# Optimization experiments

Hardware: AMD Instinct MI355X
Metric: run time of the kernel (lower is better)

Reference implementation:

```python
import jax, jax.numpy as jnp
import numpy as np

B, N, CIN, CD, NE = 64, 256, 768, 32, 8192

def setup_inputs() -> dict:
    key = jax.random.key(0)
    ks = jax.random.split(key, 8)
    z = jax.random.normal(ks[0], (B, N, CIN), dtype=jnp.float32)
    # Embedding weight: trunc_normal_(mean=0, std=1, a=-3, b=3)
    emb_weight = jax.random.truncated_normal(ks[1], -3.0, 3.0, (NE, CD)).astype(jnp.float32)
    # Linears stored as [in, out] so y = x @ W + b
    W_compress = jax.random.normal(ks[2], (CIN, CD), dtype=jnp.float32) / np.sqrt(CIN)
    b_compress = jnp.zeros((CD,), dtype=jnp.float32)
    W_ct = jax.random.normal(ks[3], (CD, CD), dtype=jnp.float32) / np.sqrt(CD)
    b_ct = jnp.zeros((CD,), dtype=jnp.float32)
    W_expand = jax.random.normal(ks[4], (CD, CIN), dtype=jnp.float32) / np.sqrt(CD)
    b_expand = jnp.zeros((CIN,), dtype=jnp.float32)
    return {"z": z, "emb_weight": emb_weight, "W_compress": W_compress,
            "b_compress": b_compress, "W_ct": W_ct, "b_ct": b_ct,
            "W_expand": W_expand, "b_expand": b_expand}

def reference(z, emb_weight, W_compress, b_compress, W_ct, b_ct, W_expand, b_expand):
    sg = jax.lax.stop_gradient
    # torch uses embedding.weight.data -> detached codebook input
    implicit_codebook = sg(emb_weight) @ W_ct + b_ct              # [NE, CD]
    zc = z @ W_compress + b_compress                              # [B, N, CD]
    z_flat = zc.reshape(-1, zc.shape[-1])                         # [B*N, CD]
    # squared distance: ||z||^2 + ||c||^2 - 2 z.c
    d = (jnp.sum(z_flat ** 2, axis=1, keepdims=True)
         + jnp.sum(implicit_codebook ** 2, axis=1)
         - 2.0 * jnp.einsum('bd,nd->bn', z_flat, implicit_codebook))  # [B*N, NE]
    indices = jnp.argmin(d, axis=1)                               # [B*N]
    z_q = implicit_codebook[indices]                              # [B*N, CD]
    # training-path losses (codebook + 2.0 * commitment)
    loss = (jnp.mean((sg(z_q) - z_flat) ** 2)
            + 2.0 * jnp.mean((z_q - sg(z_flat)) ** 2))
    # straight-through estimator
    z_st = sg(z_q) + z_flat - sg(z_flat)
    out = z_st.reshape(zc.shape) @ W_expand + b_expand            # [B, N, CIN]
    return out, loss
```

## Files before the change

kernel.cpp:

```cpp
#include <hip/hip_runtime.h>

constexpr int CIN = 768;
constexpr int CD  = 32;
constexpr int NE  = 8192;
constexpr int M   = 16384;
constexpr int SCH = 64;
constexpr int CPC = NE / SCH;
constexpr int PTB = 128;
#define MARGIN 0.05f

typedef short short8 __attribute__((ext_vector_type(8)));
typedef float f32x4  __attribute__((ext_vector_type(4)));

__device__ inline void split_bf16(float x, unsigned short& h, unsigned short& l) {
  unsigned u = __float_as_uint(x);
  unsigned hb = (u + 0x7FFFu + ((u >> 16) & 1u)) >> 16;
  float hf = __uint_as_float(hb << 16);
  float r = x - hf;
  unsigned u2 = __float_as_uint(r);
  unsigned lb = (u2 + 0x7FFFu + ((u2 >> 16) & 1u)) >> 16;
  h = (unsigned short)hb;
  l = (unsigned short)lb;
}

__device__ inline void gload_lds16(const void* g, void* l) {
  __builtin_amdgcn_global_load_lds(
      (const __attribute__((address_space(1))) unsigned int*)g,
      (__attribute__((address_space(3))) unsigned int*)l, 16, 0, 0);
}

__global__ __launch_bounds__(256) void k_split(
    const float* __restrict__ Wc, const float* __restrict__ We,
    unsigned short* __restrict__ WcTh, unsigned short* __restrict__ WcTl,
    unsigned short* __restrict__ WeTh, unsigned short* __restrict__ WeTl) {
  const int t = threadIdx.x;
  if (blockIdx.x < 96) {
    const int idx = blockIdx.x * 256 + t;
    const int k = idx >> 5, n = idx & 31;
    unsigned short h, l;
    split_bf16(Wc[idx], h, l);
    WcTh[n * CIN + k] = h;
    WcTl[n * CIN + k] = l;
  } else {
    const int idx = (blockIdx.x - 96) * 256 + t;
    const int k = idx / CIN, n = idx - k * CIN;
    unsigned short h, l;
    split_bf16(We[idx], h, l);
    WeTh[n * CD + k] = h;
    WeTl[n * CD + k] = l;
  }
}

__global__ __launch_bounds__(256) void k_main(
    const float* __restrict__ z,
    const unsigned short* __restrict__ WcTh, const unsigned short* __restrict__ WcTl,
    const float* __restrict__ bc,
    const float* __restrict__ emb, const float* __restrict__ Wct,
    const float* __restrict__ bct,
    float* __restrict__ zc, unsigned short* __restrict__ zh,
    unsigned short* __restrict__ zl,
    float* __restrict__ cb, float* __restrict__ cbT, float* __restrict__ cnorm,
    unsigned short* __restrict__ ch, unsigned short* __restrict__ cl) {
  __shared__ float smem[1632];
  const int t = threadIdx.x;
  if (blockIdx.x >= 1024) {
    for (int i = t; i < CD * CD; i += 256) smem[i] = Wct[i];
    __syncthreads();
    const int g   = (blockIdx.x - 1024) * 256 + t;
    const int row = g >> 5;
    const int col = g & 31;
    float acc = bct[col];
    const float* er = emb + row * CD;
    #pragma unroll
    for (int k = 0; k < CD; ++k) acc = fmaf(er[k], smem[k * CD + col], acc);
    cb[g] = acc;
    cbT[(long)col * NE + row] = acc;
    unsigned short h, l;
    split_bf16(acc, h, l);
    ch[g] = h; cl[g] = l;
    float v = acc * acc;
    #pragma unroll
    for (int m = 16; m >= 1; m >>= 1) v += __shfl_xor(v, m, 64);
    if (col == 0) cnorm[row] = v;
    return;
  }
  float* ps = smem;
  const int lane = t & 63;
  const int wv   = t >> 6;
  const int n    = lane & 15;
  const int quad = lane >> 4;
  const int r0   = blockIdx.x * 16;

  const float* za = z + (long)(r0 + n) * CIN + wv * 192 + quad * 8;
  const unsigned short* bh0 = WcTh + n * CIN + wv * 192 + quad * 8;
  const unsigned short* bl0 = WcTl + n * CIN + wv * 192 + quad * 8;
  const unsigned short* bh1 = bh0 + 16 * CIN;
  const unsigned short* bl1 = bl0 + 16 * CIN;

  f32x4 acc0, acc1;
  if (wv == 0) {
    const float b0 = bc[n];
    const float b1 = bc[n + 16];
    acc0 = (f32x4){b0, b0, b0, b0};
    acc1 = (f32x4){b1, b1, b1, b1};
  } else {
    acc0 = (f32x4){0.f, 0.f, 0.f, 0.f};
    acc1 = (f32x4){0.f, 0.f, 0.f, 0.f};
  }

  #pragma unroll
  for (int kt = 0; kt < 6; ++kt) {
    const float4 za0 = *(const float4*)(za + kt * 32);
    const float4 za1 = *(const float4*)(za + kt * 32 + 4);
    short8 Ah, Al;
    {
      unsigned short h, l;
      split_bf16(za0.x, h, l); Ah[0] = (short)h; Al[0] = (short)l;
      split_bf16(za0.y, h, l); Ah[1] = (short)h; Al[1] = (short)l;
      split_bf16(za0.z, h, l); Ah[2] = (short)h; Al[2] = (short)l;
      split_bf16(za0.w, h, l); Ah[3] = (short)h; Al[3] = (short)l;
      split_bf16(za1.x, h, l); Ah[4] = (short)h; Al[4] = (short)l;
      split_bf16(za1.y, h, l); Ah[5] = (short)h; Al[5] = (short)l;
      split_bf16(za1.z, h, l); Ah[6] = (short)h; Al[6] = (short)l;
      split_bf16(za1.w, h, l); Ah[7] = (short)h; Al[7] = (short)l;
    }
    const short8 Bh0 = *(const short8*)(bh0 + kt * 32);
    const short8 Bl0 = *(const short8*)(bl0 + kt * 32);
    const short8 Bh1 = *(const short8*)(bh1 + kt * 32);
    const short8 Bl1 = *(const short8*)(bl1 + kt * 32);
    acc0 = __builtin_amdgcn_mfma_f32_16x16x32_bf16(Ah, Bh0, acc0, 0, 0, 0);
    acc0 = __builtin_amdgcn_mfma_f32_16x16x32_bf16(Ah, Bl0, acc0, 0, 0, 0);
    acc0 = __builtin_amdgcn_mfma_f32_16x16x32_bf16(Al, Bh0, acc0, 0, 0, 0);
    acc1 = __builtin_amdgcn_mfma_f32_16x16x32_bf16(Ah, Bh1, acc1, 0, 0, 0);
    acc1 = __builtin_amdgcn_mfma_f32_16x16x32_bf16(Ah, Bl1, acc1, 0, 0, 0);
    acc1 = __builtin_amdgcn_mfma_f32_16x16x32_bf16(Al, Bh1, acc1, 0, 0, 0);
  }

  if (wv != 0) {
    float* pp = ps + (wv - 1) * 544;
    #pragma unroll
    for (int r = 0; r < 4; ++r) {
      const int row = quad * 4 + r;
      pp[row * 17 + n]       = acc0[r];
      pp[272 + row * 17 + n] = acc1[r];
    }
  }
  __syncthreads();
  if (wv == 0) {
    #pragma unroll
    for (int r = 0; r < 4; ++r) {
      const int row = quad * 4 + r;
      const float v0 = ((acc0[r] + ps[row * 17 + n]) + ps[544 + row * 17 + n])
                       + ps[1088 + row * 17 + n];
      const float v1 = ((acc1[r] + ps[272 + row * 17 + n]) + ps[816 + row * 17 + n])
                       + ps[1360 + row * 17 + n];
      const long i0 = (long)(r0 + row) * CD + n;
      zc[i0]      = v0;
      zc[i0 + 16] = v1;
      unsigned short h, l;
      split_bf16(-2.f * v0, h, l); zh[i0] = h;      zl[i0] = l;
      split_bf16(-2.f * v1, h, l); zh[i0 + 16] = h; zl[i0 + 16] = l;
    }
  }
}

__global__ __launch_bounds__(256) void k_argmin(
    const unsigned short* __restrict__ zh, const unsigned short* __restrict__ zl,
    const unsigned short* __restrict__ ch, const unsigned short* __restrict__ cl,
    const float* __restrict__ cnorm,
    float* __restrict__ pd) {
  __shared__ __align__(16) unsigned short chs[CPC * CD];
  __shared__ __align__(16) unsigned short cls[CPC * CD];
  const int pb   = blockIdx.x & (M / PTB - 1);
  const int cid  = blockIdx.x >> 7;
  const int lane = threadIdx.x & 63;
  const int wv   = threadIdx.x >> 6;
  const int col  = lane & 15;
  const int quad = lane >> 4;
  const int p0   = pb * PTB + wv * 32;

  const char* chg = (const char*)ch + (long)cid * (CPC * CD * 2);
  const char* clg = (const char*)cl + (long)cid * (CPC * CD * 2);
  #pragma unroll
  for (int s = 0; s < 2; ++s) {
    const int lo = s * 4096 + wv * 1024;
    gload_lds16(chg + lo + lane * 16, (char*)chs + lo);
    gload_lds16(clg + lo + lane * 16, (char*)cls + lo);
  }

  const short8 Ah0 = *(const short8*)(zh + (long)(p0 + col) * CD + quad * 8);
  const short8 Al0 = *(const short8*)(zl + (long)(p0 + col) * CD + quad * 8);
  const short8 Ah1 = *(const short8*)(zh + (long)(p0 + 16 + col) * CD + quad * 8);
  const short8 Al1 = *(const short8*)(zl + (long)(p0 + 16 + col) * CD + quad * 8);

  const int jb = cid * CPC;
  float cnv[8];
  #pragma unroll
  for (int tt = 0; tt < 8; ++tt) cnv[tt] = cnorm[jb + tt * 16 + col];

  float bd0[4], bd1[4];
  #pragma unroll
  for (int r = 0; r < 4; ++r) { bd0[r] = 1e30f; bd1[r] = 1e30f; }

  __syncthreads();

  #pragma unroll
  for (int tt = 0; tt < 8; ++tt) {
    const short8 Bh = *(const short8*)(chs + (tt * 16 + col) * CD + quad * 8);
    const short8 Bl = *(const short8*)(cls + (tt * 16 + col) * CD + quad * 8);
    const f32x4 c4 = {cnv[tt], cnv[tt], cnv[tt], cnv[tt]};
    f32x4 g0 = __builtin_amdgcn_mfma_f32_16x16x32_bf16(Ah0, Bh, c4, 0, 0, 0);
    g0 = __builtin_amdgcn_mfma_f32_16x16x32_bf16(Ah0, Bl, g0, 0, 0, 0);
    g0 = __builtin_amdgcn_mfma_f32_16x16x32_bf16(Al0, Bh, g0, 0, 0, 0);
    f32x4 g1 = __builtin_amdgcn_mfma_f32_16x16x32_bf16(Ah1, Bh, c4, 0, 0, 0);
    g1 = __builtin_amdgcn_mfma_f32_16x16x32_bf16(Ah1, Bl, g1, 0, 0, 0);
    g1 = __builtin_amdgcn_mfma_f32_16x16x32_bf16(Al1, Bh, g1, 0, 0, 0);
    #pragma unroll
    for (int r = 0; r < 4; ++r) {
      bd0[r] = fminf(bd0[r], g0[r]);
      bd1[r] = fminf(bd1[r], g1[r]);
    }
  }

  #pragma unroll
  for (int mm = 1; mm <= 8; mm <<= 1) {
    #pragma unroll
    for (int r = 0; r < 4; ++r) {
      bd0[r] = fminf(bd0[r], __shfl_xor(bd0[r], mm, 64));
      bd1[r] = fminf(bd1[r], __shfl_xor(bd1[r], mm, 64));
    }
  }
  if (col == 0) {
    #pragma unroll
    for (int r = 0; r < 4; ++r) {
      const int pA = p0 + quad * 4 + r;
      pd[(long)pA * SCH + cid] = bd0[r];
      const int pB = pA + 16;
      pd[(long)pB * SCH + cid] = bd1[r];
    }
  }
}

__global__ __launch_bounds__(256) void k_rescue(
    const float* __restrict__ zc, const float* __restrict__ cb,
    const float* __restrict__ cbT, const float* __restrict__ cnorm,
    const float* __restrict__ pd,
    float* __restrict__ zq, unsigned short* __restrict__ zqh,
    unsigned short* __restrict__ zql, float* __restrict__ lpart) {
  const int lane = threadIdx.x & 63;
  const int wv   = threadIdx.x >> 6;
  const int p    = blockIdx.x * 4 + wv;

  const float m = pd[(long)p * SCH + lane];
  float dstar = m;
  #pragma unroll
  for (int mm = 1; mm <= 32; mm <<= 1) dstar = fminf(dstar, __shfl_xor(dstar, mm, 64));
  unsigned long long mask = __ballot(m <= dstar + MARGIN);

  float zr[CD];
  {
    const float4* z4 = (const float4*)(zc + (long)p * CD);
    #pragma unroll
    for (int q = 0; q < 8; ++q) {
      float4 v = z4[q];
      zr[4 * q + 0] = v.x; zr[4 * q + 1] = v.y; zr[4 * q + 2] = v.z; zr[4 * q + 3] = v.w;
    }
  }

  float bd = 1e30f;
  int   bj = 0x7fffffff;
  while (mask) {
    const int c = (int)__builtin_ctzll(mask);
    mask &= mask - 1;
    const int j0 = c * CPC + 2 * lane;
    const float* cp = cbT + j0;
    float acc0 = 0.f, acc1 = 0.f;
    #pragma unroll
    for (int k = 0; k < CD; ++k) {
      const float2 cv = *(const float2*)(cp + (long)k * NE);
      acc0 = fmaf(zr[k], cv.x, acc0);
      acc1 = fmaf(zr[k], cv.y, acc1);
    }
    const float2 cn = *(const float2*)(cnorm + j0);
    const float d0 = fmaf(-2.f, acc0, cn.x);
    const float d1 = fmaf(-2.f, acc1, cn.y);
    if (d0 < bd) { bd = d0; bj = j0; }
    if (d1 < bd) { bd = d1; bj = j0 + 1; }
  }
  #pragma unroll
  for (int mm = 1; mm <= 32; mm <<= 1) {
    const float od = __shfl_xor(bd, mm, 64);
    const int   oj = __shfl_xor(bj, mm, 64);
    if (od < bd || (od == bd && oj < bj)) { bd = od; bj = oj; }
  }

  float ls = 0.f;
  if (lane < 32) {
    const float cv = cb[(long)bj * CD + lane];
    const float zv = zc[(long)p * CD + lane];
    zq[(long)p * CD + lane] = cv;
    unsigned short hh, ll;
    split_bf16(cv, hh, ll);
    zqh[(long)p * CD + lane] = hh;
    zql[(long)p * CD + lane] = ll;
    const float df = cv - zv;
    ls = df * df;
  }
  #pragma unroll
  for (int mm = 1; mm <= 32; mm <<= 1) ls += __shfl_xor(ls, mm, 64);
  if (lane == 0) lpart[p] = ls;
}

__global__ __launch_bounds__(256) void k_expand(
    const unsigned short* __restrict__ zqh, const unsigned short* __restrict__ zql,
    const unsigned short* __restrict__ WeTh, const unsigned short* __restrict__ WeTl,
    const float* __restrict__ be,
    const float* __restrict__ lpart,
    float* __restrict__ out,
    float* __restrict__ out_loss) {
  __shared__ double redd[4];
  const int t = threadIdx.x;
  if (blockIdx.x == 1024) {
    double v = 0.0;
    for (int k = t; k < M; k += 256) v += (double)lpart[k];
    #pragma unroll
    for (int mm = 1; mm <= 32; mm <<= 1) v += __shfl_xor(v, mm, 64);
    if ((t & 63) == 0) redd[t >> 6] = v;
    __syncthreads();
    if (t == 0)
      out_loss[0] = (float)(3.0 * (redd[0] + redd[1] + redd[2] + redd[3]) / (double)(M * CD));
    return;
  }
  const int lane = t & 63;
  const int wv   = t >> 6;
  const int col  = lane & 15;
  const int quad = lane >> 4;
  const int r0   = blockIdx.x * 16;

  const short8 Ah = *(const short8*)(zqh + (long)(r0 + col) * CD + quad * 8);
  const short8 Al = *(const short8*)(zql + (long)(r0 + col) * CD + quad * 8);

  #pragma unroll
  for (int tt = 0; tt < 12; ++tt) {
    const int n0 = (wv * 12 + tt) * 16;
    const short8 Bh = *(const short8*)(WeTh + (long)(n0 + col) * CD + quad * 8);
    const short8 Bl = *(const short8*)(WeTl + (long)(n0 + col) * CD + quad * 8);
    const float bv = be[n0 + col];
    const f32x4 c4 = {bv, bv, bv, bv};
    f32x4 g = __builtin_amdgcn_mfma_f32_16x16x32_bf16(Ah, Bh, c4, 0, 0, 0);
    g = __builtin_amdgcn_mfma_f32_16x16x32_bf16(Ah, Bl, g, 0, 0, 0);
    g = __builtin_amdgcn_mfma_f32_16x16x32_bf16(Al, Bh, g, 0, 0, 0);
    #pragma unroll
    for (int r = 0; r < 4; ++r)
      out[(long)(r0 + quad * 4 + r) * CIN + n0 + col] = g[r];
  }
}

extern "C" void kernel_launch(void* const* d_in, const int* in_sizes, int n_in,
                              void* d_out, int out_size, void* d_ws, size_t ws_size,
                              hipStream_t stream) {
  const float* z   = (const float*)d_in[0];
  const float* emb = (const float*)d_in[1];
  const float* Wc  = (const float*)d_in[2];
  const float* bc  = (const float*)d_in[3];
  const float* Wct = (const float*)d_in[4];
  const float* bct = (const float*)d_in[5];
  const float* We  = (const float*)d_in[6];
  const float* be  = (const float*)d_in[7];
  float* out = (float*)d_out;

  float* cb    = (float*)d_ws;
  float* cnorm = cb + NE * CD;
  float* zc    = cnorm + NE;
  float* zq    = zc + M * CD;
  float* pd    = zq + M * CD;
  float* lpart = pd + (long)M * SCH;
  unsigned short* zh   = (unsigned short*)(lpart + M);
  unsigned short* zl   = zh + M * CD;
  unsigned short* ch   = zl + M * CD;
  unsigned short* cl   = ch + NE * CD;
  unsigned short* zqh  = cl + NE * CD;
  unsigned short* zql  = zqh + M * CD;
  unsigned short* WeTh = zql + M * CD;
  unsigned short* WeTl = WeTh + CIN * CD;
  unsigned short* WcTh = WeTl + CIN * CD;
  unsigned short* WcTl = WcTh + CIN * CD;
  float* cbT = (float*)(WcTl + CIN * CD);

  k_split<<<192, 256, 0, stream>>>(Wc, We, WcTh, WcTl, WeTh, WeTl);
  k_main<<<2048, 256, 0, stream>>>(z, WcTh, WcTl, bc, emb, Wct, bct,
                                   zc, zh, zl, cb, cbT, cnorm, ch, cl);
  k_argmin<<<(M / PTB) * SCH, 256, 0, stream>>>(zh, zl, ch, cl, cnorm, pd);
  k_rescue<<<M / 4, 256, 0, stream>>>(zc, cb, cbT, cnorm, pd, zq, zqh, zql, lpart);
  k_expand<<<1024 + 1, 256, 0, stream>>>(zqh, zql, WeTh, WeTl, be, lpart,
                                         out, out + (long)M * CIN);
}
```

Measured before the change: 202.5 us.

## Fuse rescue and expand kernels, keep z_q in shared memory, atomic loss reduction

```diff
diff --git a/kernel.cpp b/kernel.cpp
--- a/kernel.cpp
+++ b/kernel.cpp
@@ -60,10 +60,12 @@
     float* __restrict__ zc, unsigned short* __restrict__ zh,
     unsigned short* __restrict__ zl,
     float* __restrict__ cb, float* __restrict__ cbT, float* __restrict__ cnorm,
-    unsigned short* __restrict__ ch, unsigned short* __restrict__ cl) {
+    unsigned short* __restrict__ ch, unsigned short* __restrict__ cl,
+    double* __restrict__ dacc, unsigned int* __restrict__ dcnt) {
   __shared__ float smem[1632];
   const int t = threadIdx.x;
   if (blockIdx.x >= 1024) {
+    if (blockIdx.x == 2047 && t == 0) { dacc[0] = 0.0; dcnt[0] = 0u; }
     for (int i = t; i < CD * CD; i += 256) smem[i] = Wct[i];
     __syncthreads();
     const int g   = (blockIdx.x - 1024) * 256 + t;
@@ -241,108 +243,96 @@
   }
 }
 
-__global__ __launch_bounds__(256) void k_rescue(
+__global__ __launch_bounds__(512) void k_fin(
     const float* __restrict__ zc, const float* __restrict__ cb,
     const float* __restrict__ cbT, const float* __restrict__ cnorm,
     const float* __restrict__ pd,
-    float* __restrict__ zq, unsigned short* __restrict__ zqh,
-    unsigned short* __restrict__ zql, float* __restrict__ lpart) {
-  const int lane = threadIdx.x & 63;
-  const int wv   = threadIdx.x >> 6;
-  const int p    = blockIdx.x * 4 + wv;
-
-  const float m = pd[(long)p * SCH + lane];
-  float dstar = m;
-  #pragma unroll
-  for (int mm = 1; mm <= 32; mm <<= 1) dstar = fminf(dstar, __shfl_xor(dstar, mm, 64));
-  unsigned long long mask = __ballot(m <= dstar + MARGIN);
-
-  float zr[CD];
-  {
-    const float4* z4 = (const float4*)(zc + (long)p * CD);
-    #pragma unroll
-    for (int q = 0; q < 8; ++q) {
-      float4 v = z4[q];
-      zr[4 * q + 0] = v.x; zr[4 * q + 1] = v.y; zr[4 * q + 2] = v.z; zr[4 * q + 3] = v.w;
-    }
-  }
-
-  float bd = 1e30f;
-  int   bj = 0x7fffffff;
-  while (mask) {
-    const int c = (int)__builtin_ctzll(mask);
-    mask &= mask - 1;
-    const int j0 = c * CPC + 2 * lane;
-    const float* cp = cbT + j0;
-    float acc0 = 0.f, acc1 = 0.f;
-    #pragma unroll
-    for (int k = 0; k < CD; ++k) {
-      const float2 cv = *(const float2*)(cp + (long)k * NE);
-      acc0 = fmaf(zr[k], cv.x, acc0);
-      acc1 = fmaf(zr[k], cv.y, acc1);
-    }
-    const float2 cn = *(const float2*)(cnorm + j0);
-    const float d0 = fmaf(-2.f, acc0, cn.x);
-    const float d1 = fmaf(-2.f, acc1, cn.y);
-    if (d0 < bd) { bd = d0; bj = j0; }
-    if (d1 < bd) { bd = d1; bj = j0 + 1; }
-  }
-  #pragma unroll
-  for (int mm = 1; mm <= 32; mm <<= 1) {
-    const float od = __shfl_xor(bd, mm, 64);
-    const int   oj = __shfl_xor(bj, mm, 64);
-    if (od < bd || (od == bd && oj < bj)) { bd = od; bj = oj; }
-  }
-
-  float ls = 0.f;
-  if (lane < 32) {
-    const float cv = cb[(long)bj * CD + lane];
-    const float zv = zc[(long)p * CD + lane];
-    zq[(long)p * CD + lane] = cv;
-    unsigned short hh, ll;
-    split_bf16(cv, hh, ll);
-    zqh[(long)p * CD + lane] = hh;
-    zql[(long)p * CD + lane] = ll;
-    const float df = cv - zv;
-    ls = df * df;
-  }
-  #pragma unroll
-  for (int mm = 1; mm <= 32; mm <<= 1) ls += __shfl_xor(ls, mm, 64);
-  if (lane == 0) lpart[p] = ls;
-}
-
-__global__ __launch_bounds__(256) void k_expand(
-    const unsigned short* __restrict__ zqh, const unsigned short* __restrict__ zql,
     const unsigned short* __restrict__ WeTh, const unsigned short* __restrict__ WeTl,
     const float* __restrict__ be,
-    const float* __restrict__ lpart,
-    float* __restrict__ out,
-    float* __restrict__ out_loss) {
-  __shared__ double redd[4];
-  const int t = threadIdx.x;
-  if (blockIdx.x == 1024) {
-    double v = 0.0;
-    for (int k = t; k < M; k += 256) v += (double)lpart[k];
-    #pragma unroll
-    for (int mm = 1; mm <= 32; mm <<= 1) v += __shfl_xor(v, mm, 64);
-    if ((t & 63) == 0) redd[t >> 6] = v;
-    __syncthreads();
-    if (t == 0)
-      out_loss[0] = (float)(3.0 * (redd[0] + redd[1] + redd[2] + redd[3]) / (double)(M * CD));
-    return;
-  }
+    float* __restrict__ out, float* __restrict__ out_loss,
+    double* __restrict__ dacc, unsigned int* __restrict__ dcnt) {
+  __shared__ float zqs[16][33];
+  __shared__ float lls[8];
+  const int t    = threadIdx.x;
   const int lane = t & 63;
   const int wv   = t >> 6;
+  const int r0   = blockIdx.x * 16;
+
+  float wls = 0.f;
+  for (int i = 0; i < 2; ++i) {
+    const int row = wv * 2 + i;
+    const int p   = r0 + row;
+
+    const float m = pd[(long)p * SCH + lane];
+    float dstar = m;
+    #pragma unroll
+    for (int mm = 1; mm <= 32; mm <<= 1) dstar = fminf(dstar, __shfl_xor(dstar, mm, 64));
+    unsigned long long mask = __ballot(m <= dstar + MARGIN);
+
+    float zr[CD];
+    {
+      const float4* z4 = (const float4*)(zc + (long)p * CD);
+      #pragma unroll
+      for (int q = 0; q < 8; ++q) {
+        float4 v = z4[q];
+        zr[4 * q + 0] = v.x; zr[4 * q + 1] = v.y; zr[4 * q + 2] = v.z; zr[4 * q + 3] = v.w;
+      }
+    }
+
+    float bd = 1e30f;
+    int   bj = 0x7fffffff;
+    while (mask) {
+      const int c = (int)__builtin_ctzll(mask);
+      mask &= mask - 1;
+      const int j0 = c * CPC + 2 * lane;
+      const float* cp = cbT + j0;
+      float acc0 = 0.f, acc1 = 0.f;
+      #pragma unroll
+      for (int k = 0; k < CD; ++k) {
+        const float2 cv = *(const float2*)(cp + (long)k * NE);
+        acc0 = fmaf(zr[k], cv.x, acc0);
+        acc1 = fmaf(zr[k], cv.y, acc1);
+      }
+      const float2 cn = *(const float2*)(cnorm + j0);
+      const float d0 = fmaf(-2.f, acc0, cn.x);
+      const float d1 = fmaf(-2.f, acc1, cn.y);
+      if (d0 < bd) { bd = d0; bj = j0; }
+      if (d1 < bd) { bd = d1; bj = j0 + 1; }
+    }
+    #pragma unroll
+    for (int mm = 1; mm <= 32; mm <<= 1) {
+      const float od = __shfl_xor(bd, mm, 64);
+      const int   oj = __shfl_xor(bj, mm, 64);
+      if (od < bd || (od == bd && oj < bj)) { bd = od; bj = oj; }
+    }
+
+    float ls = 0.f;
+    if (lane < 32) {
+      const float cv = cb[(long)bj * CD + lane];
+      const float zv = zc[(long)p * CD + lane];
+      zqs[row][lane] = cv;
+      const float df = cv - zv;
+      ls = df * df;
+    }
+    #pragma unroll
+    for (int mm = 1; mm <= 32; mm <<= 1) ls += __shfl_xor(ls, mm, 64);
+    wls += ls;
+  }
+  if (lane == 0) lls[wv] = wls;
+  __syncthreads();
+
   const int col  = lane & 15;
   const int quad = lane >> 4;
-  const int r0   = blockIdx.x * 16;
-
-  const short8 Ah = *(const short8*)(zqh + (long)(r0 + col) * CD + quad * 8);
-  const short8 Al = *(const short8*)(zql + (long)(r0 + col) * CD + quad * 8);
-
-  #pragma unroll
-  for (int tt = 0; tt < 12; ++tt) {
-    const int n0 = (wv * 12 + tt) * 16;
+  short8 Ah, Al;
+  #pragma unroll
+  for (int j = 0; j < 8; ++j) {
+    unsigned short h, l;
+    split_bf16(zqs[col][quad * 8 + j], h, l);
+    Ah[j] = (short)h; Al[j] = (short)l;
+  }
+  #pragma unroll
+  for (int tt = 0; tt < 6; ++tt) {
+    const int n0 = (wv * 6 + tt) * 16;
     const short8 Bh = *(const short8*)(WeTh + (long)(n0 + col) * CD + quad * 8);
     const short8 Bl = *(const short8*)(WeTl + (long)(n0 + col) * CD + quad * 8);
     const float bv = be[n0 + col];
@@ -353,6 +343,19 @@
     #pragma unroll
     for (int r = 0; r < 4; ++r)
       out[(long)(r0 + quad * 4 + r) * CIN + n0 + col] = g[r];
+  }
+
+  if (t == 0) {
+    double bsum = 0.0;
+    #pragma unroll
+    for (int w = 0; w < 8; ++w) bsum += (double)lls[w];
+    atomicAdd(dacc, bsum);
+    __threadfence();
+    const unsigned v = atomicAdd(dcnt, 1u);
+    if (v == 1023u) {
+      const double s = atomicAdd(dacc, 0.0);
+      out_loss[0] = (float)(3.0 * s / (double)(M * CD));
+    }
   }
 }
 
@@ -372,26 +375,23 @@
   float* cb    = (float*)d_ws;
   float* cnorm = cb + NE * CD;
   float* zc    = cnorm + NE;
-  float* zq    = zc + M * CD;
-  float* pd    = zq + M * CD;
-  float* lpart = pd + (long)M * SCH;
-  unsigned short* zh   = (unsigned short*)(lpart + M);
+  float* pd    = zc + M * CD;
+  unsigned short* zh   = (unsigned short*)(pd + (long)M * SCH);
   unsigned short* zl   = zh + M * CD;
   unsigned short* ch   = zl + M * CD;
   unsigned short* cl   = ch + NE * CD;
-  unsigned short* zqh  = cl + NE * CD;
-  unsigned short* zql  = zqh + M * CD;
-  unsigned short* WeTh = zql + M * CD;
+  unsigned short* WeTh = cl + NE * CD;
   unsigned short* WeTl = WeTh + CIN * CD;
   unsigned short* WcTh = WeTl + CIN * CD;
   unsigned short* WcTl = WcTh + CIN * CD;
   float* cbT = (float*)(WcTl + CIN * CD);
+  double* dacc = (double*)(cbT + (long)CD * NE);
+  unsigned int* dcnt = (unsigned int*)(dacc + 1);
 
   k_split<<<192, 256, 0, stream>>>(Wc, We, WcTh, WcTl, WeTh, WeTl);
   k_main<<<2048, 256, 0, stream>>>(z, WcTh, WcTl, bc, emb, Wct, bct,
-                                   zc, zh, zl, cb, cbT, cnorm, ch, cl);
+                                   zc, zh, zl, cb, cbT, cnorm, ch, cl, dacc, dcnt);
   k_argmin<<<(M / PTB) * SCH, 256, 0, stream>>>(zh, zl, ch, cl, cnorm, pd);
-  k_rescue<<<M / 4, 256, 0, stream>>>(zc, cb, cbT, cnorm, pd, zq, zqh, zql, lpart);
-  k_expand<<<1024 + 1, 256, 0, stream>>>(zqh, zql, WeTh, WeTl, be, lpart,
-                                         out, out + (long)M * CIN);
-}
+  k_fin<<<M / 16, 512, 0, stream>>>(zc, cb, cbT, cnorm, pd, WeTh, WeTl, be,
+                                    out, out + (long)M * CIN, dacc, dcnt);
+}
```

New measurement: 223.7 us. 1.1x slower.

## Double argmin rows per block and stage expand output through LDS for vector stores

Applied to the files above, without the earlier changes.

```diff
diff --git a/kernel.cpp b/kernel.cpp
--- a/kernel.cpp
+++ b/kernel.cpp
@@ -6,7 +6,7 @@
 constexpr int M   = 16384;
 constexpr int SCH = 64;
 constexpr int CPC = NE / SCH;
-constexpr int PTB = 128;
+constexpr int PTB = 256;
 #define MARGIN 0.05f
 
 typedef short short8 __attribute__((ext_vector_type(8)));
@@ -172,12 +172,12 @@
   __shared__ __align__(16) unsigned short chs[CPC * CD];
   __shared__ __align__(16) unsigned short cls[CPC * CD];
   const int pb   = blockIdx.x & (M / PTB - 1);
-  const int cid  = blockIdx.x >> 7;
+  const int cid  = blockIdx.x >> 6;
   const int lane = threadIdx.x & 63;
   const int wv   = threadIdx.x >> 6;
   const int col  = lane & 15;
   const int quad = lane >> 4;
-  const int p0   = pb * PTB + wv * 32;
+  const int p0   = pb * PTB + wv * 64;
 
   const char* chg = (const char*)ch + (long)cid * (CPC * CD * 2);
   const char* clg = (const char*)cl + (long)cid * (CPC * CD * 2);
@@ -188,19 +188,23 @@
     gload_lds16(clg + lo + lane * 16, (char*)cls + lo);
   }
 
-  const short8 Ah0 = *(const short8*)(zh + (long)(p0 + col) * CD + quad * 8);
-  const short8 Al0 = *(const short8*)(zl + (long)(p0 + col) * CD + quad * 8);
-  const short8 Ah1 = *(const short8*)(zh + (long)(p0 + 16 + col) * CD + quad * 8);
-  const short8 Al1 = *(const short8*)(zl + (long)(p0 + 16 + col) * CD + quad * 8);
+  short8 Ah[4], Al[4];
+  #pragma unroll
+  for (int s = 0; s < 4; ++s) {
+    Ah[s] = *(const short8*)(zh + (long)(p0 + s * 16 + col) * CD + quad * 8);
+    Al[s] = *(const short8*)(zl + (long)(p0 + s * 16 + col) * CD + quad * 8);
+  }
 
   const int jb = cid * CPC;
   float cnv[8];
   #pragma unroll
   for (int tt = 0; tt < 8; ++tt) cnv[tt] = cnorm[jb + tt * 16 + col];
 
-  float bd0[4], bd1[4];
-  #pragma unroll
-  for (int r = 0; r < 4; ++r) { bd0[r] = 1e30f; bd1[r] = 1e30f; }
+  float bd[4][4];
+  #pragma unroll
+  for (int s = 0; s < 4; ++s)
+    #pragma unroll
+    for (int r = 0; r < 4; ++r) bd[s][r] = 1e30f;
 
   __syncthreads();
 
@@ -209,35 +213,32 @@
     const short8 Bh = *(const short8*)(chs + (tt * 16 + col) * CD + quad * 8);
     const short8 Bl = *(const short8*)(cls + (tt * 16 + col) * CD + quad * 8);
     const f32x4 c4 = {cnv[tt], cnv[tt], cnv[tt], cnv[tt]};
-    f32x4 g0 = __builtin_amdgcn_mfma_f32_16x16x32_bf16(Ah0, Bh, c4, 0, 0, 0);
-    g0 = __builtin_amdgcn_mfma_f32_16x16x32_bf16(Ah0, Bl, g0, 0, 0, 0);
-    g0 = __builtin_amdgcn_mfma_f32_16x16x32_bf16(Al0, Bh, g0, 0, 0, 0);
-    f32x4 g1 = __builtin_amdgcn_mfma_f32_16x16x32_bf16(Ah1, Bh, c4, 0, 0, 0);
-    g1 = __builtin_amdgcn_mfma_f32_16x16x32_bf16(Ah1, Bl, g1, 0, 0, 0);
-    g1 = __builtin_amdgcn_mfma_f32_16x16x32_bf16(Al1, Bh, g1, 0, 0, 0);
-    #pragma unroll
-    for (int r = 0; r < 4; ++r) {
-      bd0[r] = fminf(bd0[r], g0[r]);
-      bd1[r] = fminf(bd1[r], g1[r]);
+    #pragma unroll
+    for (int s = 0; s < 4; ++s) {
+      f32x4 g = __builtin_amdgcn_mfma_f32_16x16x32_bf16(Ah[s], Bh, c4, 0, 0, 0);
+      g = __builtin_amdgcn_mfma_f32_16x16x32_bf16(Ah[s], Bl, g, 0, 0, 0);
+      g = __builtin_amdgcn_mfma_f32_16x16x32_bf16(Al[s], Bh, g, 0, 0, 0);
+      #pragma unroll
+      for (int r = 0; r < 4; ++r) bd[s][r] = fminf(bd[s][r], g[r]);
     }
   }
 
   #pragma unroll
   for (int mm = 1; mm <= 8; mm <<= 1) {
     #pragma unroll
-    for (int r = 0; r < 4; ++r) {
-      bd0[r] = fminf(bd0[r], __shfl_xor(bd0[r], mm, 64));
-      bd1[r] = fminf(bd1[r], __shfl_xor(bd1[r], mm, 64));
-    }
+    for (int s = 0; s < 4; ++s)
+      #pragma unroll
+      for (int r = 0; r < 4; ++r)
+        bd[s][r] = fminf(bd[s][r], __shfl_xor(bd[s][r], mm, 64));
   }
   if (col == 0) {
     #pragma unroll
-    for (int r = 0; r < 4; ++r) {
-      const int pA = p0 + quad * 4 + r;
-      pd[(long)pA * SCH + cid] = bd0[r];
-      const int pB = pA + 16;
-      pd[(long)pB * SCH + cid] = bd1[r];
-    }
+    for (int s = 0; s < 4; ++s)
+      #pragma unroll
+      for (int r = 0; r < 4; ++r) {
+        const int pA = p0 + s * 16 + quad * 4 + r;
+        pd[(long)pA * SCH + cid] = bd[s][r];
+      }
   }
 }
 
@@ -318,6 +319,7 @@
     const float* __restrict__ lpart,
     float* __restrict__ out,
     float* __restrict__ out_loss) {
+  __shared__ float ob[16][388];
   __shared__ double redd[4];
   const int t = threadIdx.x;
   if (blockIdx.x == 1024) {
@@ -340,19 +342,35 @@
   const short8 Ah = *(const short8*)(zqh + (long)(r0 + col) * CD + quad * 8);
   const short8 Al = *(const short8*)(zql + (long)(r0 + col) * CD + quad * 8);
 
-  #pragma unroll
-  for (int tt = 0; tt < 12; ++tt) {
-    const int n0 = (wv * 12 + tt) * 16;
-    const short8 Bh = *(const short8*)(WeTh + (long)(n0 + col) * CD + quad * 8);
-    const short8 Bl = *(const short8*)(WeTl + (long)(n0 + col) * CD + quad * 8);
-    const float bv = be[n0 + col];
-    const f32x4 c4 = {bv, bv, bv, bv};
-    f32x4 g = __builtin_amdgcn_mfma_f32_16x16x32_bf16(Ah, Bh, c4, 0, 0, 0);
-    g = __builtin_amdgcn_mfma_f32_16x16x32_bf16(Ah, Bl, g, 0, 0, 0);
-    g = __builtin_amdgcn_mfma_f32_16x16x32_bf16(Al, Bh, g, 0, 0, 0);
-    #pragma unroll
-    for (int r = 0; r < 4; ++r)
-      out[(long)(r0 + quad * 4 + r) * CIN + n0 + col] = g[r];
+  for (int g2 = 0; g2 < 2; ++g2) {
+    #pragma unroll
+    for (int ttl = 0; ttl < 6; ++ttl) {
+      const int tt = g2 * 6 + ttl;
+      const int n0 = (wv * 12 + tt) * 16;
+      const short8 Bh = *(const short8*)(WeTh + (long)(n0 + col) * CD + quad * 8);
+      const short8 Bl = *(const short8*)(WeTl + (long)(n0 + col) * CD + quad * 8);
+      const float bv = be[n0 + col];
+      const f32x4 c4 = {bv, bv, bv, bv};
+      f32x4 g = __builtin_amdgcn_mfma_f32_16x16x32_bf16(Ah, Bh, c4, 0, 0, 0);
+      g = __builtin_amdgcn_mfma_f32_16x16x32_bf16(Ah, Bl, g, 0, 0, 0);
+      g = __builtin_amdgcn_mfma_f32_16x16x32_bf16(Al, Bh, g, 0, 0, 0);
+      #pragma unroll
+      for (int r = 0; r < 4; ++r)
+        ob[quad * 4 + r][wv * 96 + ttl * 16 + col] = g[r];
+    }
+    __syncthreads();
+    #pragma unroll
+    for (int i = 0; i < 6; ++i) {
+      const int f    = t + i * 256;
+      const int row  = f / 96;
+      const int lc4  = f - row * 96;
+      const int strp = lc4 / 24;
+      const int c4in = lc4 - strp * 24;
+      const int cg4  = strp * 48 + g2 * 24 + c4in;
+      *(float4*)(out + (long)(r0 + row) * CIN + cg4 * 4) =
+          *(const float4*)(&ob[row][lc4 * 4]);
+    }
+    __syncthreads();
   }
 }
 
```

New measurement: 196.8 us. -2.8%, faster.
